# Kernel tuning notes

Measured on AMD Instinct MI355X. Metric: run time of the kernel, lower is better.

Reference implementation:

```python
import jax, jax.numpy as jnp
import numpy as np

N_NODES = 50000
N_EDGES = 800000
IN_DIM = 64
OUT_DIM = 64
EDGE_DIM = 16
LN_EPS = 1e-5


def setup_inputs() -> dict:
    key = jax.random.key(0)
    ks = jax.random.split(key, 12)
    def lin(k, fan_in, fan_out):
        # torch nn.Linear default init: U(-1/sqrt(fan_in), 1/sqrt(fan_in))
        kw, kb = jax.random.split(k)
        bound = 1.0 / np.sqrt(fan_in)
        W = jax.random.uniform(kw, (fan_in, fan_out), jnp.float32, -bound, bound)
        b = jax.random.uniform(kb, (fan_out,), jnp.float32, -bound, bound)
        return W, b
    x = jax.random.normal(ks[0], (N_NODES, IN_DIM), jnp.float32)
    edge_index = jax.random.randint(ks[1], (2, N_EDGES), 0, N_NODES, jnp.int64 if jax.config.jax_enable_x64 else jnp.int32)
    edge_features = jax.random.normal(ks[2], (N_EDGES, EDGE_DIM), jnp.float32)
    W1, b1 = lin(ks[3], IN_DIM + EDGE_DIM, OUT_DIM)   # msg_mlp layer 1
    W2, b2 = lin(ks[4], OUT_DIM, OUT_DIM)             # msg_mlp layer 2
    W3, b3 = lin(ks[5], IN_DIM + OUT_DIM, OUT_DIM)    # update_mlp
    gamma = jnp.ones((OUT_DIM,), jnp.float32)
    beta = jnp.zeros((OUT_DIM,), jnp.float32)
    return {"x": x, "edge_index": edge_index, "edge_features": edge_features,
            "W1": W1, "b1": b1, "W2": W2, "b2": b2, "W3": W3, "b3": b3,
            "gamma": gamma, "beta": beta}


def reference(x, edge_index, edge_features, W1, b1, W2, b2, W3, b3, gamma, beta):
    num_nodes = x.shape[0]
    src, dst = edge_index[0], edge_index[1]
    # gather source node feats, concat with edge feats -> message MLP
    msg_in = jnp.concatenate([x[src], edge_features], axis=-1)           # [E, in+edge]
    h = jax.nn.relu(msg_in @ W1 + b1)
    messages = h @ W2 + b2                                               # [E, out]
    # scatter-add aggregate + mean by in-degree (count + 1e-8)
    agg = jax.ops.segment_sum(messages, dst, num_segments=num_nodes)     # [N, out]
    cnt = jax.ops.segment_sum(jnp.ones((messages.shape[0],), x.dtype), dst,
                              num_segments=num_nodes)[:, None]           # [N, 1]
    agg = agg / (cnt + 1e-8)
    # update MLP + residual (Identity since in_dim == out_dim) + LayerNorm
    updated = jax.nn.relu(jnp.concatenate([x, agg], axis=-1) @ W3 + b3)  # [N, out]
    y = updated + x
    mu = jnp.mean(y, axis=-1, keepdims=True)
    var = jnp.var(y, axis=-1, keepdims=True)
    return (y - mu) * jax.lax.rsqrt(var + LN_EPS) * gamma + beta
```

## Files before the change

kernel.cpp:

```cpp
#include <hip/hip_runtime.h>

typedef unsigned short u16;
typedef unsigned int u32;
typedef short short8 __attribute__((ext_vector_type(8)));
typedef short short4v __attribute__((ext_vector_type(4)));
typedef float floatx4 __attribute__((ext_vector_type(4)));

#define NE 800000
#define NNODES 50000
#define NBLK 196

#define EDGE_GRID 1536

#define LDS_FENCE() __asm__ volatile("s_waitcnt lgkmcnt(0)" ::: "memory")

__device__ __forceinline__ u16 f2bf(float f) {
    union { float f; unsigned int i; } v; v.f = f;
    return (u16)((v.i + 0x7fffu + ((v.i >> 16) & 1u)) >> 16);
}
__device__ __forceinline__ u32 f2bf2(float lo, float hi) {
    u32 r;
    asm("v_cvt_pk_bf16_f32 %0, %1, %2" : "=v"(r) : "v"(lo), "v"(hi));
    return r;
}
__device__ __forceinline__ float bf2f(u16 u) {
    union { unsigned int i; float f; } v; v.i = ((unsigned int)u) << 16; return v.f;
}
__device__ __forceinline__ short8 pack8(const float4 a, const float4 b) {
    union { short8 s; u32 u[4]; } o;
    o.u[0] = f2bf2(a.x, a.y);
    o.u[1] = f2bf2(a.z, a.w);
    o.u[2] = f2bf2(b.x, b.y);
    o.u[3] = f2bf2(b.z, b.w);
    return o.s;
}
__device__ __forceinline__ short8 ld8_bf(const float* __restrict__ p) {
    return pack8(*(const float4*)p, *(const float4*)(p + 4));
}

#define MFMA16(a, b, c) __builtin_amdgcn_mfma_f32_16x16x32_bf16(a, b, c, 0, 0, 0)

__global__ __launch_bounds__(256) void prep_kernel(
    const float* __restrict__ x, const int* __restrict__ ei,
    int* __restrict__ hist, u16* __restrict__ xbf, float* __restrict__ agg)
{
    const int id = blockIdx.x * 256 + threadIdx.x;
    if (id < NE) {
        atomicAdd(&hist[ei[NE + id]], 1);
        float4 z; z.x = 0.f; z.y = 0.f; z.z = 0.f; z.w = 0.f;
        *(float4*)&agg[(size_t)id * 4] = z;
    }
    if (id < NNODES * 8) {
        *(short8*)&xbf[(size_t)id * 8] = ld8_bf(x + (size_t)id * 8);
    }
}

__global__ __launch_bounds__(256) void scan1_kernel(
    const int* __restrict__ hist, int* __restrict__ cursor, int* __restrict__ bsum)
{
    const int i = blockIdx.x * 256 + threadIdx.x;
    const int lane = threadIdx.x & 63;
    const int w = threadIdx.x >> 6;
    const int v = (i < NNODES) ? hist[i] : 0;
    int inc = v;
    #pragma unroll
    for (int o = 1; o < 64; o <<= 1) {
        const int tt = __shfl_up(inc, o);
        if (lane >= o) inc += tt;
    }
    __shared__ int ws[4];
    if (lane == 63) ws[w] = inc;
    __syncthreads();
    int add = 0;
    for (int j = 0; j < w; ++j) add += ws[j];
    const int excl = inc - v + add;
    if (i < NNODES) cursor[i] = excl;
    if (threadIdx.x == 255) bsum[blockIdx.x] = excl + v;
}

__global__ __launch_bounds__(256) void scatter_kernel(
    const int* __restrict__ ei, int* __restrict__ cursor,
    const int* __restrict__ bsum, uint2* __restrict__ sde)
{
    __shared__ int bsx[256];
    __shared__ int ws[4];
    {
        const int tid = threadIdx.x;
        const int lane = tid & 63;
        const int w = tid >> 6;
        const int v = (tid < NBLK) ? bsum[tid] : 0;
        int inc = v;
        #pragma unroll
        for (int o = 1; o < 64; o <<= 1) {
            const int tt = __shfl_up(inc, o);
            if (lane >= o) inc += tt;
        }
        if (lane == 63) ws[w] = inc;
        __syncthreads();
        int add = 0;
        for (int j = 0; j < w; ++j) add += ws[j];
        bsx[tid] = inc - v + add;
    }
    __syncthreads();

    const int e = blockIdx.x * 256 + threadIdx.x;
    if (e < NE) {
        const int dst = ei[NE + e];
        const int p = atomicAdd(&cursor[dst], 1) + bsx[dst >> 8];
        uint2 v;
        v.x = (u32)e;
        v.y = ((u32)ei[e] << 16) | (u32)dst;
        sde[p] = v;
    }
}

__global__ __launch_bounds__(256) void edge_kernel(
    const u16* __restrict__ xbf, const float* __restrict__ ef,
    const float* __restrict__ w1, const float* __restrict__ b1,
    const float* __restrict__ w2, const float* __restrict__ b2,
    const uint2* __restrict__ sde, float* __restrict__ agg)
{
    constexpr int S1 = 104;
    constexpr int SM = 20;
    __shared__ u16 A1[4][16 * S1];
    __shared__ u16 W2f[2][4][64 * 8];

    const int wid  = threadIdx.x >> 6;
    const int lane = threadIdx.x & 63;
    const int q    = lane >> 4;
    const int c    = lane & 15;
    const int r4   = lane >> 2;
    const int p4   = lane & 3;

    short8 w1f[3][4];
    #pragma unroll
    for (int kk = 0; kk < 3; ++kk)
        #pragma unroll
        for (int nn = 0; nn < 4; ++nn)
            #pragma unroll
            for (int j = 0; j < 8; ++j) {
                const int k = kk * 32 + q * 8 + j;
                float wv;
                if (k < 80)       wv = w1[k * 64 + nn * 16 + c];
                else if (k == 80) wv = b1[nn * 16 + c];
                else              wv = 0.f;
                w1f[kk][nn][j] = (short)f2bf(wv);
            }
    if (wid == 0) {
        #pragma unroll
        for (int kk = 0; kk < 2; ++kk)
            #pragma unroll
            for (int nn = 0; nn < 4; ++nn) {
                short8 f;
                #pragma unroll
                for (int j = 0; j < 8; ++j) {
                    const int k = kk * 32 + q * 8 + j;
                    f[j] = (short)f2bf(w2[k * 64 + nn * 16 + c]);
                }
                *(short8*)&W2f[kk][nn][lane * 8] = f;
            }
    }
    float b2v[4];
    #pragma unroll
    for (int nn = 0; nn < 4; ++nn) b2v[nn] = b2[nn * 16 + c];
    __syncthreads();

    const floatx4 zero = {0.f, 0.f, 0.f, 0.f};
    const int ntile = NE / 16;
    const int stride = gridDim.x * 4;
    int t = blockIdx.x * 4 + wid;

    uint2 sdB; u32 eB;
    short8 xa, xb; float4 ev;
    int dcur;
    {
        const uint2 sdA = sde[t * 16 + c];
        const u32  eA  = sde[t * 16 + r4].x;
        dcur = (int)(sdA.y & 0xffffu);
        const int sA = (int)(sdA.y >> 16);
        int tb = t + stride; if (tb >= ntile) tb = ntile - 1;
        sdB = sde[tb * 16 + c];
        eB  = sde[tb * 16 + r4].x;
        const u16* xp = xbf + (size_t)sA * 64 + q * 16;
        xa = *(const short8*)xp;
        xb = *(const short8*)(xp + 8);
        ev = *(const float4*)(ef + (size_t)eA * 16 + p4 * 4);
    }

    for (; t < ntile; t += stride) {
        u16* arow = &A1[wid][c * S1 + q * 16];
        *(short8*)arow       = xa;
        *(short8*)(arow + 8) = xb;
        {
            short4v e4;
            e4[0] = (short)f2bf(ev.x); e4[1] = (short)f2bf(ev.y);
            e4[2] = (short)f2bf(ev.z); e4[3] = (short)f2bf(ev.w);
            *(short4v*)&A1[wid][r4 * S1 + 64 + p4 * 4] = e4;
        }
        if (q == 1) {
            short8 zb = {0, 0, 0, 0, 0, 0, 0, 0};
            zb[0] = (short)0x3F80;
            *(short8*)&A1[wid][c * S1 + 80] = zb;
            const short8 z8 = {0, 0, 0, 0, 0, 0, 0, 0};
            *(short8*)&A1[wid][c * S1 + 88] = z8;
        }
        LDS_FENCE();

        short8 a1k[3];
        #pragma unroll
        for (int kk = 0; kk < 3; ++kk)
            a1k[kk] = *(const short8*)&A1[wid][c * S1 + kk * 32 + q * 8];

        const int dnext = (int)(sdB.y & 0xffffu);
        {
            const int sN = (int)(sdB.y >> 16);
            const u16* xp = xbf + (size_t)sN * 64 + q * 16;
            xa = *(const short8*)xp;
            xb = *(const short8*)(xp + 8);
            ev = *(const float4*)(ef + (size_t)eB * 16 + p4 * 4);
        }
        {
            int tb = t + 2 * stride; if (tb >= ntile) tb = ntile - 1;
            sdB = sde[tb * 16 + c];
            eB  = sde[tb * 16 + r4].x;
        }

        #pragma unroll
        for (int nn = 0; nn < 4; ++nn) {
            floatx4 acc = MFMA16(w1f[0][nn], a1k[0], zero);
            acc = MFMA16(w1f[1][nn], a1k[1], acc);
            acc = MFMA16(w1f[2][nn], a1k[2], acc);
            uint2 pv;
            pv.x = f2bf2(fmaxf(acc[0], 0.f), fmaxf(acc[1], 0.f));
            pv.y = f2bf2(fmaxf(acc[2], 0.f), fmaxf(acc[3], 0.f));
            *(uint2*)&A1[wid][c * S1 + nn * 16 + q * 4] = pv;
        }
        LDS_FENCE();

        short8 a2k[2];
        #pragma unroll
        for (int kk = 0; kk < 2; ++kk)
            a2k[kk] = *(const short8*)&A1[wid][c * S1 + kk * 32 + q * 8];

        #pragma unroll
        for (int nn = 0; nn < 4; ++nn) {
            const short8 wf0 = *(const short8*)&W2f[0][nn][lane * 8];
            const short8 wf1 = *(const short8*)&W2f[1][nn][lane * 8];
            floatx4 mg = MFMA16(a2k[0], wf0, zero);
            mg = MFMA16(a2k[1], wf1, mg);
            uint2 pv;
            pv.x = f2bf2(mg[0] + b2v[nn], mg[1] + b2v[nn]);
            pv.y = f2bf2(mg[2] + b2v[nn], mg[3] + b2v[nn]);
            *(uint2*)&A1[wid][(nn * 16 + c) * SM + q * 4] = pv;
        }
        LDS_FENCE();

        const uint2 ma = *(const uint2*)&A1[wid][lane * SM];
        const uint2 mb = *(const uint2*)&A1[wid][lane * SM + 4];
        const uint2 mc = *(const uint2*)&A1[wid][lane * SM + 8];
        const uint2 md = *(const uint2*)&A1[wid][lane * SM + 12];
        const u32 w_[8] = {ma.x, ma.y, mb.x, mb.y, mc.x, mc.y, md.x, md.y};
        int dc = __shfl(dcur, 0);
        float acc = bf2f((u16)(w_[0] & 0xffffu));
        #pragma unroll
        for (int row = 1; row < 16; ++row) {
            const int d = __shfl(dcur, row);
            const float v = bf2f((u16)((w_[row >> 1] >> ((row & 1) * 16)) & 0xffffu));
            if (d == dc) {
                acc += v;
            } else {
                atomicAdd(&agg[(size_t)dc * 64 + lane], acc);
                dc = d;
                acc = v;
            }
        }
        atomicAdd(&agg[(size_t)dc * 64 + lane], acc);

        dcur = dnext;
    }
}

__global__ __launch_bounds__(256) void node_kernel(
    const u16* __restrict__ xbf, const float* __restrict__ w3,
    const float* __restrict__ b3, const float* __restrict__ g,
    const float* __restrict__ bb, const float* __restrict__ agg,
    const int* __restrict__ hist, float* __restrict__ out)
{
    constexpr int S3 = 136;
    __shared__ u16 Cs[4][16 * S3];

    const int wid  = threadIdx.x >> 6;
    const int lane = threadIdx.x & 63;
    const int q    = lane >> 4;
    const int c    = lane & 15;

    short8 w3f[4][4];
    #pragma unroll
    for (int kk = 0; kk < 4; ++kk)
        #pragma unroll
        for (int nn = 0; nn < 4; ++nn)
            #pragma unroll
            for (int j = 0; j < 8; ++j) {
                const int k = kk * 32 + q * 8 + j;
                w3f[kk][nn][j] = (short)f2bf(w3[k * 64 + nn * 16 + c]);
            }
    float b3v[4], gv[4], bv[4];
    #pragma unroll
    for (int nn = 0; nn < 4; ++nn) {
        b3v[nn] = b3[nn * 16 + c];
        gv[nn]  = g[nn * 16 + c];
        bv[nn]  = bb[nn * 16 + c];
    }

    const floatx4 zero = {0.f, 0.f, 0.f, 0.f};
    const int ntile = NNODES / 16;

    for (int t = blockIdx.x * 4 + wid; t < ntile; t += gridDim.x * 4) {
        const int n0 = t * 16;
        const int node = n0 + c;
        u16* crow = &Cs[wid][c * S3];

        if (q < 2) {
            const u16* xp = xbf + (size_t)node * 64 + q * 32;
            *(short8*)&crow[q * 32]      = *(const short8*)xp;
            *(short8*)&crow[q * 32 + 8]  = *(const short8*)(xp + 8);
            *(short8*)&crow[q * 32 + 16] = *(const short8*)(xp + 16);
            *(short8*)&crow[q * 32 + 24] = *(const short8*)(xp + 24);
        } else {
            const int p = q - 2;
            const float inv = 1.0f / ((float)hist[node] + 1e-8f);
            const float* ap = agg + (size_t)node * 64 + p * 32;
            #pragma unroll
            for (int gi = 0; gi < 4; ++gi) {
                const float4 v0 = *(const float4*)(ap + gi * 8);
                const float4 v1 = *(const float4*)(ap + gi * 8 + 4);
                union { short8 s; u32 u[4]; } o;
                o.u[0] = f2bf2(v0.x * inv, v0.y * inv);
                o.u[1] = f2bf2(v0.z * inv, v0.w * inv);
                o.u[2] = f2bf2(v1.x * inv, v1.y * inv);
                o.u[3] = f2bf2(v1.z * inv, v1.w * inv);
                *(short8*)&crow[64 + p * 32 + gi * 8] = o.s;
            }
        }
        LDS_FENCE();

        short8 af[4];
        #pragma unroll
        for (int kk = 0; kk < 4; ++kk)
            af[kk] = *(const short8*)&Cs[wid][c * S3 + kk * 32 + q * 8];

        float y[4][4];
        float s[4]  = {0.f, 0.f, 0.f, 0.f};
        float ss[4] = {0.f, 0.f, 0.f, 0.f};
        #pragma unroll
        for (int nn = 0; nn < 4; ++nn) {
            floatx4 acc = MFMA16(af[0], w3f[0][nn], zero);
            acc = MFMA16(af[1], w3f[1][nn], acc);
            acc = MFMA16(af[2], w3f[2][nn], acc);
            acc = MFMA16(af[3], w3f[3][nn], acc);
            #pragma unroll
            for (int r = 0; r < 4; ++r) {
                const float upd = fmaxf(acc[r] + b3v[nn], 0.f);
                const float xv = bf2f(Cs[wid][(q * 4 + r) * S3 + nn * 16 + c]);
                const float yy = upd + xv;
                y[r][nn] = yy;
                s[r] += yy;
                ss[r] += yy * yy;
            }
        }

        #pragma unroll
        for (int r = 0; r < 4; ++r) {
            float sr = s[r], sq = ss[r];
            #pragma unroll
            for (int off = 1; off < 16; off <<= 1) {
                sr += __shfl_xor(sr, off);
                sq += __shfl_xor(sq, off);
            }
            const float mu  = sr * (1.0f / 64.0f);
            const float var = sq * (1.0f / 64.0f) - mu * mu;
            const float rs  = rsqrtf(var + 1e-5f);
            float* op = out + (size_t)(n0 + q * 4 + r) * 64 + c;
            #pragma unroll
            for (int nn = 0; nn < 4; ++nn)
                op[nn * 16] = (y[r][nn] - mu) * rs * gv[nn] + bv[nn];
        }
    }
}

extern "C" void kernel_launch(void* const* d_in, const int* in_sizes, int n_in,
                              void* d_out, int out_size, void* d_ws, size_t ws_size,
                              hipStream_t stream) {
    const float* x   = (const float*)d_in[0];
    const int*   ei  = (const int*)d_in[1];
    const float* ef  = (const float*)d_in[2];
    const float* w1  = (const float*)d_in[3];
    const float* b1  = (const float*)d_in[4];
    const float* w2  = (const float*)d_in[5];
    const float* b2  = (const float*)d_in[6];
    const float* w3  = (const float*)d_in[7];
    const float* b3  = (const float*)d_in[8];
    const float* g   = (const float*)d_in[9];
    const float* bb  = (const float*)d_in[10];

    float* agg   = (float*)d_ws;
    int* hist    = (int*)d_ws + 3200000;
    int* cursor  = hist + NNODES;
    int* bsum    = cursor + NNODES;
    int* bsumx   = bsum + 256;
    u16* xbf     = (u16*)(bsumx + 256);
    uint2* sde   = (uint2*)((int*)d_ws + 4900512);

    hipMemsetAsync(hist, 0, (size_t)NNODES * sizeof(int), stream);
    prep_kernel<<<3125, 256, 0, stream>>>(x, ei, hist, xbf, agg);
    scan1_kernel<<<NBLK, 256, 0, stream>>>(hist, cursor, bsum);
    scatter_kernel<<<3125, 256, 0, stream>>>(ei, cursor, bsum, sde);
    edge_kernel<<<EDGE_GRID, 256, 0, stream>>>(xbf, ef, w1, b1, w2, b2, sde, agg);
    node_kernel<<<782, 256, 0, stream>>>(xbf, w3, b3, g, bb, agg, hist, (float*)d_out);
}
```

Before: 269.7 us.

## Replace per-edge global atomic scatter with two-level bucket binning and LDS sort

The per-edge scatter, which did one global atomic on a per-node cursor for every edge, is replaced by two stages. First, each block bins 2048 edges by 256-node bucket using LDS atomics and claims space with a single global atomic per bucket. Then a per-bucket kernel counting-sorts that bucket's records by the low 8 bits of dst in LDS and writes them back. This is meant to cut contended random global atomics and scattered writes, at the cost of an extra launch and an extra read/write pass over the sorted edge array. Buckets larger than CHUNK_CAP are left unsorted, which could break correctness on skewed inputs.

```diff
diff --git a/kernel.cpp b/kernel.cpp
--- a/kernel.cpp
+++ b/kernel.cpp
@@ -9,6 +9,9 @@
 #define NE 800000
 #define NNODES 50000
 #define NBLK 196
+#define BIN_EDGES 2048
+#define BIN_GRID 391
+#define CHUNK_CAP 5120
 
 #define EDGE_GRID 1536
 
@@ -56,7 +59,7 @@
 }
 
 __global__ __launch_bounds__(256) void scan1_kernel(
-    const int* __restrict__ hist, int* __restrict__ cursor, int* __restrict__ bsum)
+    const int* __restrict__ hist, int* __restrict__ bsum)
 {
     const int i = blockIdx.x * 256 + threadIdx.x;
     const int lane = threadIdx.x & 63;
@@ -73,19 +76,22 @@
     __syncthreads();
     int add = 0;
     for (int j = 0; j < w; ++j) add += ws[j];
-    const int excl = inc - v + add;
-    if (i < NNODES) cursor[i] = excl;
-    if (threadIdx.x == 255) bsum[blockIdx.x] = excl + v;
-}
-
-__global__ __launch_bounds__(256) void scatter_kernel(
-    const int* __restrict__ ei, int* __restrict__ cursor,
-    const int* __restrict__ bsum, uint2* __restrict__ sde)
+    if (threadIdx.x == 255) bsum[blockIdx.x] = inc + add;
+}
+
+__global__ __launch_bounds__(256) void bin_kernel(
+    const int* __restrict__ ei, const int* __restrict__ bsum,
+    int* __restrict__ ccur, uint2* __restrict__ sde)
 {
+    __shared__ u16 dstv[BIN_EDGES];
+    __shared__ u16 srcv[BIN_EDGES];
+    __shared__ int h[NBLK];
+    __shared__ int basev[NBLK];
     __shared__ int bsx[256];
     __shared__ int ws[4];
+
+    const int tid = threadIdx.x;
     {
-        const int tid = threadIdx.x;
         const int lane = tid & 63;
         const int w = tid >> 6;
         const int v = (tid < NBLK) ? bsum[tid] : 0;
@@ -96,6 +102,7 @@
             if (lane >= o) inc += tt;
         }
         if (lane == 63) ws[w] = inc;
+        if (tid < NBLK) h[tid] = 0;
         __syncthreads();
         int add = 0;
         for (int j = 0; j < w; ++j) add += ws[j];
@@ -103,15 +110,101 @@
     }
     __syncthreads();
 
-    const int e = blockIdx.x * 256 + threadIdx.x;
-    if (e < NE) {
-        const int dst = ei[NE + e];
-        const int p = atomicAdd(&cursor[dst], 1) + bsx[dst >> 8];
+    const int e0 = blockIdx.x * BIN_EDGES;
+    const int n = (NE - e0 < BIN_EDGES) ? (NE - e0) : BIN_EDGES;
+
+    for (int i = tid; i < n; i += 256) {
+        const int d = ei[NE + e0 + i];
+        const int s = ei[e0 + i];
+        dstv[i] = (u16)d;
+        srcv[i] = (u16)s;
+        atomicAdd(&h[d >> 8], 1);
+    }
+    __syncthreads();
+
+    if (tid < NBLK) {
+        const int cnt = h[tid];
+        int r = 0;
+        if (cnt > 0) r = atomicAdd(&ccur[tid], cnt);
+        basev[tid] = bsx[tid] + r;
+        h[tid] = 0;
+    }
+    __syncthreads();
+
+    for (int i = tid; i < n; i += 256) {
+        const int d = dstv[i];
+        const int kb = d >> 8;
+        const int rank = atomicAdd(&h[kb], 1);
         uint2 v;
-        v.x = (u32)e;
-        v.y = ((u32)ei[e] << 16) | (u32)dst;
-        sde[p] = v;
-    }
+        v.x = (u32)(e0 + i);
+        v.y = ((u32)srcv[i] << 16) | (u32)d;
+        sde[basev[kb] + rank] = v;
+    }
+}
+
+__global__ __launch_bounds__(256) void sortchunk_kernel(
+    const int* __restrict__ bsum, uint2* __restrict__ sde)
+{
+    __shared__ uint2 rec[CHUNK_CAP];
+    __shared__ int h[256];
+    __shared__ int bsx[256];
+    __shared__ int ws[4];
+
+    const int tid = threadIdx.x;
+    {
+        const int lane = tid & 63;
+        const int w = tid >> 6;
+        const int v = (tid < NBLK) ? bsum[tid] : 0;
+        int inc = v;
+        #pragma unroll
+        for (int o = 1; o < 64; o <<= 1) {
+            const int tt = __shfl_up(inc, o);
+            if (lane >= o) inc += tt;
+        }
+        if (lane == 63) ws[w] = inc;
+        h[tid] = 0;
+        __syncthreads();
+        int add = 0;
+        for (int j = 0; j < w; ++j) add += ws[j];
+        bsx[tid] = inc - v + add;
+    }
+    __syncthreads();
+
+    const int B = bsx[blockIdx.x];
+    const int N = bsum[blockIdx.x];
+    if (N > CHUNK_CAP) return;
+
+    for (int i = tid; i < N; i += 256)
+        atomicAdd(&h[sde[B + i].y & 255], 1);
+    __syncthreads();
+
+    {
+        const int lane = tid & 63;
+        const int w = tid >> 6;
+        const int v = h[tid];
+        int inc = v;
+        #pragma unroll
+        for (int o = 1; o < 64; o <<= 1) {
+            const int tt = __shfl_up(inc, o);
+            if (lane >= o) inc += tt;
+        }
+        if (lane == 63) ws[w] = inc;
+        __syncthreads();
+        int add = 0;
+        for (int j = 0; j < w; ++j) add += ws[j];
+        h[tid] = inc - v + add;
+    }
+    __syncthreads();
+
+    for (int i = tid; i < N; i += 256) {
+        const uint2 r = sde[B + i];
+        const int pos = atomicAdd(&h[r.y & 255], 1);
+        rec[pos] = r;
+    }
+    __syncthreads();
+
+    for (int i = tid; i < N; i += 256)
+        sde[B + i] = rec[i];
 }
 
 __global__ __launch_bounds__(256) void edge_kernel(
@@ -410,11 +503,13 @@
     int* bsumx   = bsum + 256;
     u16* xbf     = (u16*)(bsumx + 256);
     uint2* sde   = (uint2*)((int*)d_ws + 4900512);
-
-    hipMemsetAsync(hist, 0, (size_t)NNODES * sizeof(int), stream);
+    (void)bsumx;
+
+    hipMemsetAsync(hist, 0, (size_t)(NNODES + 256) * sizeof(int), stream);
     prep_kernel<<<3125, 256, 0, stream>>>(x, ei, hist, xbf, agg);
-    scan1_kernel<<<NBLK, 256, 0, stream>>>(hist, cursor, bsum);
-    scatter_kernel<<<3125, 256, 0, stream>>>(ei, cursor, bsum, sde);
+    scan1_kernel<<<NBLK, 256, 0, stream>>>(hist, bsum);
+    bin_kernel<<<BIN_GRID, 256, 0, stream>>>(ei, bsum, cursor, sde);
+    sortchunk_kernel<<<NBLK, 256, 0, stream>>>(bsum, sde);
     edge_kernel<<<EDGE_GRID, 256, 0, stream>>>(xbf, ef, w1, b1, w2, b2, sde, agg);
     node_kernel<<<782, 256, 0, stream>>>(xbf, w3, b3, g, bb, agg, hist, (float*)d_out);
 }
```

New measurement: 237.8 us. 11.9% less time.
